# Kernel optimization log

Measured on AMD Instinct MI355X. Metric: run time of the kernel, lower is better.

The kernel has to match this reference:

```python
import jax, jax.numpy as jnp
import numpy as np

HID, FFN, NE, TOPK = 1024, 4096, 8, 2


def setup_inputs() -> dict:
    key = jax.random.key(0)
    ks = jax.random.split(key, 4)
    x = jax.random.normal(ks[0], (2, 2048, HID), dtype=jnp.float32)
    # router: nn.Linear(hidden, num_experts, bias=False), init std=0.02; stored as [H, E]
    Wr = jax.random.normal(ks[1], (HID, NE), dtype=jnp.float32) * 0.02
    # per-expert FFN weights stacked on leading expert axis
    W1 = jax.random.normal(ks[2], (NE, HID, FFN), dtype=jnp.float32) * (1.0 / np.sqrt(HID))
    b1 = jnp.zeros((NE, FFN), dtype=jnp.float32)
    W2 = jax.random.normal(ks[3], (NE, FFN, HID), dtype=jnp.float32) * (1.0 / np.sqrt(FFN))
    b2 = jnp.zeros((NE, HID), dtype=jnp.float32)
    return {"x": x, "Wr": Wr, "W1": W1, "b1": b1, "W2": W2, "b2": b2}


def reference(x, Wr, W1, b1, W2, b2):
    B, S, H = x.shape
    E = Wr.shape[1]
    T = B * S
    xf = x.reshape(T, H)                                  # [T, H]
    logits = xf @ Wr                                      # [T, E]
    probs = jax.nn.softmax(logits, axis=-1)
    topk_p, topk_i = jax.lax.top_k(probs, TOPK)           # [T, K]
    topk_p = topk_p / jnp.sum(topk_p, axis=-1, keepdims=True)
    # dense combine weights: c[t, e] = normalized prob if expert e selected for token t else 0
    c = jnp.zeros((T, E), dtype=xf.dtype).at[jnp.arange(T)[:, None], topk_i].add(topk_p)

    def expert_step(acc, ew):
        w1, bb1, w2, bb2, ce = ew                         # ce: [T]
        h = jax.nn.gelu(xf @ w1 + bb1, approximate=False)  # exact GELU like nn.GELU()
        y = h @ w2 + bb2                                  # [T, H]
        return acc + ce[:, None] * y, None

    out, _ = jax.lax.scan(expert_step, jnp.zeros_like(xf), (W1, b1, W2, b2, c.T))
    return out.reshape(B, S, H)
```

## Files before the change

### kernel.cpp

```cpp
#include <hip/hip_runtime.h>
#include <hip/hip_bf16.h>

#define H 1024
#define F 4096
#define NE 8
#define T 4096

typedef unsigned short u16;
typedef float floatx4 __attribute__((ext_vector_type(4)));
typedef short short8 __attribute__((ext_vector_type(8)));

__device__ __forceinline__ u16 f2bf(float f) {
  union { float f; unsigned int u; } c; c.f = f;
  unsigned int u = c.u;
  return (u16)((u + 0x7fffu + ((u >> 16) & 1u)) >> 16);
}

__device__ __forceinline__ void load16_lds(const u16* g, u16* l) {
  __builtin_amdgcn_global_load_lds(
      (const __attribute__((address_space(1))) unsigned int*)g,
      (__attribute__((address_space(3))) unsigned int*)l, 16, 0, 0);
}

__global__ __launch_bounds__(256) void router_kernel(
    const float* __restrict__ x, const float* __restrict__ Wr,
    int* __restrict__ cnt, int* __restrict__ tok, float* __restrict__ wgt) {
  int t = (blockIdx.x * 256 + threadIdx.x) >> 6;
  int lane = threadIdx.x & 63;
  const float* xr = x + (size_t)t * H;
  double p[NE];
#pragma unroll
  for (int e = 0; e < NE; ++e) p[e] = 0.0;
  for (int k = lane; k < H; k += 64) {
    float xv = xr[k];
    const float4* wr4 = reinterpret_cast<const float4*>(Wr + k * NE);
    float4 a = wr4[0], b = wr4[1];
    p[0] += (double)xv * a.x; p[1] += (double)xv * a.y;
    p[2] += (double)xv * a.z; p[3] += (double)xv * a.w;
    p[4] += (double)xv * b.x; p[5] += (double)xv * b.y;
    p[6] += (double)xv * b.z; p[7] += (double)xv * b.w;
  }
#pragma unroll
  for (int e = 0; e < NE; ++e) {
#pragma unroll
    for (int off = 32; off; off >>= 1) p[e] += __shfl_down(p[e], off, 64);
  }
  if (lane == 0) {
    int i0 = 0;
#pragma unroll
    for (int e = 1; e < NE; ++e) if (p[e] > p[i0]) i0 = e;
    int i1 = (i0 == 0) ? 1 : 0;
#pragma unroll
    for (int e = 0; e < NE; ++e) if (e != i0 && p[e] > p[i1]) i1 = e;
    double d = exp(p[i1] - p[i0]);
    float w0 = (float)(1.0 / (1.0 + d));
    float w1 = (float)(d / (1.0 + d));
    int pos0 = atomicAdd(&cnt[i0], 1);
    tok[i0 * T + pos0] = t; wgt[i0 * T + pos0] = w0;
    int pos1 = atomicAdd(&cnt[i1], 1);
    tok[i1 * T + pos1] = t; wgt[i1 * T + pos1] = w1;
  }
}

__global__ void offsets_kernel(const int* __restrict__ cnt, int* __restrict__ off) {
  if (threadIdx.x == 0) {
    int s = 0;
#pragma unroll
    for (int e = 0; e < NE; ++e) { off[e] = s; s += cnt[e]; }
    off[NE] = s;
  }
}

__global__ __launch_bounds__(256) void convert_x_kernel(
    const float* __restrict__ x, u16* __restrict__ xb) {
  int i = blockIdx.x * 256 + threadIdx.x;
  float4 v = reinterpret_cast<const float4*>(x)[i];
  ushort4 o;
  o.x = f2bf(v.x); o.y = f2bf(v.y); o.z = f2bf(v.z); o.w = f2bf(v.w);
  reinterpret_cast<ushort4*>(xb)[i] = o;
}

__global__ __launch_bounds__(256) void transpose_bf16_kernel(
    const float* __restrict__ src, u16* __restrict__ dst, int R, int C) {
  __shared__ u16 tile[64][72];
  int e = blockIdx.z;
  int c0 = blockIdx.x << 6, r0 = blockIdx.y << 6;
  const float* s = src + (size_t)e * R * C;
  u16* d = dst + (size_t)e * R * C;
  int t = threadIdx.x;
  int rl = t >> 4, cl = (t & 15) << 2;
#pragma unroll
  for (int i = 0; i < 4; ++i) {
    float4 v = *reinterpret_cast<const float4*>(&s[(size_t)(r0 + rl + i * 16) * C + c0 + cl]);
    ushort4 o; o.x = f2bf(v.x); o.y = f2bf(v.y); o.z = f2bf(v.z); o.w = f2bf(v.w);
    *reinterpret_cast<ushort4*>(&tile[rl + i * 16][cl]) = o;
  }
  __syncthreads();
  int cl2 = t >> 4, rl2 = (t & 15) << 2;
#pragma unroll
  for (int i = 0; i < 4; ++i) {
    ushort4 o;
    o.x = tile[rl2 + 0][cl2 + i * 16];
    o.y = tile[rl2 + 1][cl2 + i * 16];
    o.z = tile[rl2 + 2][cl2 + i * 16];
    o.w = tile[rl2 + 3][cl2 + i * 16];
    *reinterpret_cast<ushort4*>(&d[(size_t)(c0 + cl2 + i * 16) * R + r0 + rl2]) = o;
  }
}

__global__ __launch_bounds__(256) void gemm1_kernel(
    const u16* __restrict__ Xb, const u16* __restrict__ W1t,
    const float* __restrict__ b1, const int* __restrict__ cnt,
    const int* __restrict__ off, const int* __restrict__ tok,
    u16* __restrict__ Hc) {
  int e = blockIdx.z;
  int n = cnt[e];
  int m0 = blockIdx.y << 7;
  if (m0 >= n) return;
  int n0 = blockIdx.x << 7;
  int rb = off[e];

  __shared__ alignas(16) u16 As[128 * 32];
  __shared__ alignas(16) u16 Bs[128 * 32];
  __shared__ int tokS[128];

  int tid = threadIdx.x;
  if (tid < 128) {
    int s = m0 + tid;
    tokS[tid] = (s < n) ? tok[e * T + s] : 0;
  }
  __syncthreads();

  const u16* W1e = W1t + (size_t)e * F * H;
  const u16* aP0 = Xb + (size_t)tokS[tid >> 2] * H + (tid & 3) * 8;
  const u16* aP1 = Xb + (size_t)tokS[64 + (tid >> 2)] * H + (tid & 3) * 8;
  const u16* bP0 = W1e + (size_t)(n0 + (tid >> 2)) * H + (tid & 3) * 8;
  const u16* bP1 = W1e + (size_t)(n0 + 64 + (tid >> 2)) * H + (tid & 3) * 8;
  u16* aL0 = &As[tid * 8];        u16* aL1 = &As[(tid + 256) * 8];
  u16* bL0 = &Bs[tid * 8];        u16* bL1 = &Bs[(tid + 256) * 8];

  int wv = tid >> 6, lane = tid & 63;
  int wm = wv >> 1, wn = wv & 1;
  int quad = lane >> 4, l16 = lane & 15;

  floatx4 acc[4][4];
#pragma unroll
  for (int mt = 0; mt < 4; ++mt)
#pragma unroll
    for (int nt = 0; nt < 4; ++nt) acc[mt][nt] = floatx4{0.f, 0.f, 0.f, 0.f};

  const u16* aF[4]; const u16* bF[4];
#pragma unroll
  for (int i = 0; i < 4; ++i) {
    aF[i] = &As[(wm * 64 + i * 16 + l16) * 32 + quad * 8];
    bF[i] = &Bs[(wn * 64 + i * 16 + l16) * 32 + quad * 8];
  }

  for (int k0 = 0; k0 < H; k0 += 32) {
    load16_lds(aP0 + k0, aL0);
    load16_lds(aP1 + k0, aL1);
    load16_lds(bP0 + k0, bL0);
    load16_lds(bP1 + k0, bL1);
    __syncthreads();
    short8 av[4], bv[4];
#pragma unroll
    for (int i = 0; i < 4; ++i) {
      av[i] = *reinterpret_cast<const short8*>(aF[i]);
      bv[i] = *reinterpret_cast<const short8*>(bF[i]);
    }
#pragma unroll
    for (int mt = 0; mt < 4; ++mt)
#pragma unroll
      for (int nt = 0; nt < 4; ++nt)
        acc[mt][nt] = __builtin_amdgcn_mfma_f32_16x16x32_bf16(av[mt], bv[nt], acc[mt][nt], 0, 0, 0);
    __syncthreads();
  }

  float b1v[4];
#pragma unroll
  for (int nt = 0; nt < 4; ++nt)
    b1v[nt] = b1[e * F + n0 + wn * 64 + nt * 16 + l16];
#pragma unroll
  for (int mt = 0; mt < 4; ++mt) {
#pragma unroll
    for (int i = 0; i < 4; ++i) {
      int row = wm * 64 + mt * 16 + quad * 4 + i;
      int gr = m0 + row;
      if (gr < n) {
        u16* hrow = Hc + (size_t)(rb + gr) * F + n0 + wn * 64 + l16;
#pragma unroll
        for (int nt = 0; nt < 4; ++nt) {
          float v = acc[mt][nt][i] + b1v[nt];
          v = 0.5f * v * (1.0f + erff(v * 0.70710678118f));
          hrow[nt * 16] = f2bf(v);
        }
      }
    }
  }
}

__global__ __launch_bounds__(256) void gemm2_kernel(
    const u16* __restrict__ Hc, const u16* __restrict__ W2t,
    const float* __restrict__ b2, const int* __restrict__ cnt,
    const int* __restrict__ off, const int* __restrict__ tok,
    const float* __restrict__ wgt, float* __restrict__ out) {
  int e = blockIdx.z;
  int n = cnt[e];
  int m0 = blockIdx.y << 7;
  if (m0 >= n) return;
  int n0 = blockIdx.x << 7;
  int rb = off[e];

  __shared__ alignas(16) u16 As[128 * 32];
  __shared__ alignas(16) u16 Bs[128 * 32];

  int tid = threadIdx.x;
  const u16* W2e = W2t + (size_t)e * F * H;
  const u16* aP0 = Hc + (size_t)(rb + m0 + (tid >> 2)) * F + (tid & 3) * 8;
  const u16* aP1 = Hc + (size_t)(rb + m0 + 64 + (tid >> 2)) * F + (tid & 3) * 8;
  const u16* bP0 = W2e + (size_t)(n0 + (tid >> 2)) * F + (tid & 3) * 8;
  const u16* bP1 = W2e + (size_t)(n0 + 64 + (tid >> 2)) * F + (tid & 3) * 8;
  u16* aL0 = &As[tid * 8];        u16* aL1 = &As[(tid + 256) * 8];
  u16* bL0 = &Bs[tid * 8];        u16* bL1 = &Bs[(tid + 256) * 8];

  int wv = tid >> 6, lane = tid & 63;
  int wm = wv >> 1, wn = wv & 1;
  int quad = lane >> 4, l16 = lane & 15;

  floatx4 acc[4][4];
#pragma unroll
  for (int mt = 0; mt < 4; ++mt)
#pragma unroll
    for (int nt = 0; nt < 4; ++nt) acc[mt][nt] = floatx4{0.f, 0.f, 0.f, 0.f};

  const u16* aF[4]; const u16* bF[4];
#pragma unroll
  for (int i = 0; i < 4; ++i) {
    aF[i] = &As[(wm * 64 + i * 16 + l16) * 32 + quad * 8];
    bF[i] = &Bs[(wn * 64 + i * 16 + l16) * 32 + quad * 8];
  }

  for (int k0 = 0; k0 < F; k0 += 32) {
    load16_lds(aP0 + k0, aL0);
    load16_lds(aP1 + k0, aL1);
    load16_lds(bP0 + k0, bL0);
    load16_lds(bP1 + k0, bL1);
    __syncthreads();
    short8 av[4], bv[4];
#pragma unroll
    for (int i = 0; i < 4; ++i) {
      av[i] = *reinterpret_cast<const short8*>(aF[i]);
      bv[i] = *reinterpret_cast<const short8*>(bF[i]);
    }
#pragma unroll
    for (int mt = 0; mt < 4; ++mt)
#pragma unroll
      for (int nt = 0; nt < 4; ++nt)
        acc[mt][nt] = __builtin_amdgcn_mfma_f32_16x16x32_bf16(av[mt], bv[nt], acc[mt][nt], 0, 0, 0);
    __syncthreads();
  }

  float b2v[4];
#pragma unroll
  for (int nt = 0; nt < 4; ++nt)
    b2v[nt] = b2[e * H + n0 + wn * 64 + nt * 16 + l16];
#pragma unroll
  for (int mt = 0; mt < 4; ++mt) {
#pragma unroll
    for (int i = 0; i < 4; ++i) {
      int row = wm * 64 + mt * 16 + quad * 4 + i;
      int gr = m0 + row;
      if (gr < n) {
        float wv2 = wgt[e * T + gr];
        int tk = tok[e * T + gr];
        float* orow = out + (size_t)tk * H + n0 + wn * 64 + l16;
#pragma unroll
        for (int nt = 0; nt < 4; ++nt)
          atomicAdd(orow + nt * 16, (acc[mt][nt][i] + b2v[nt]) * wv2);
      }
    }
  }
}

extern "C" void kernel_launch(void* const* d_in, const int* in_sizes, int n_in,
                              void* d_out, int out_size, void* d_ws, size_t ws_size,
                              hipStream_t stream) {
  const float* x  = (const float*)d_in[0];
  const float* Wr = (const float*)d_in[1];
  const float* W1 = (const float*)d_in[2];
  const float* b1 = (const float*)d_in[3];
  const float* W2 = (const float*)d_in[4];
  const float* b2 = (const float*)d_in[5];
  float* out = (float*)d_out;

  char* ws = (char*)d_ws;
  int*   cnt = (int*)(ws + 0);
  int*   off = (int*)(ws + 256);
  int*   tok = (int*)(ws + 4096);
  float* wgt = (float*)(ws + 135168);
  u16*   Xb  = (u16*)(ws + 266240);
  u16*   W1t = (u16*)(ws + 8654848);
  u16*   W2t = (u16*)(ws + 75763712);
  u16*   Hc  = (u16*)(ws + 142872576);

  hipMemsetAsync(cnt, 0, 64, stream);
  hipMemsetAsync(out, 0, (size_t)out_size * sizeof(float), stream);

  router_kernel<<<dim3(T / 4), dim3(256), 0, stream>>>(x, Wr, cnt, tok, wgt);
  offsets_kernel<<<dim3(1), dim3(64), 0, stream>>>(cnt, off);
  convert_x_kernel<<<dim3((T * H / 4) / 256), dim3(256), 0, stream>>>(x, Xb);
  transpose_bf16_kernel<<<dim3(F / 64, H / 64, NE), dim3(256), 0, stream>>>(W1, W1t, H, F);
  transpose_bf16_kernel<<<dim3(H / 64, F / 64, NE), dim3(256), 0, stream>>>(W2, W2t, F, H);
  gemm1_kernel<<<dim3(F / 128, 32, NE), dim3(256), 0, stream>>>(Xb, W1t, b1, cnt, off, tok, Hc);
  gemm2_kernel<<<dim3(H / 128, 32, NE), dim3(256), 0, stream>>>(Hc, W2t, b2, cnt, off, tok, wgt, out);
}
```

Baseline: 699.5 us.

## Fuse x conversion into router, stage GEMM1 stores via LDS, split-K GEMM2

Converting x to bf16 now happens inside the router kernel, so the separate convert launch is gone. GEMM1's epilogue uses a tanh-style GELU approximation (sigmoid form with __expf and rcp) and writes its output through an LDS tile, which gives coalesced 16-byte stores instead of scattered 2-byte ones. GEMM2 splits K into two halves across grid z to double the block count, and both halves atomically add into the output. The GELU approximation departs from the exact erf form, and the split-K doubles the atomic traffic on the output.

```diff
diff --git a/kernel.cpp b/kernel.cpp
--- a/kernel.cpp
+++ b/kernel.cpp
@@ -16,6 +16,13 @@
   return (u16)((u + 0x7fffu + ((u >> 16) & 1u)) >> 16);
 }
 
+__device__ __forceinline__ float gelu_f(float x) {
+  float x3 = x * x * x;
+  float m2y = -1.5957691216f * x - 0.0713548162f * x3;
+  float u = __expf(m2y);
+  return x * __builtin_amdgcn_rcpf(1.0f + u);
+}
+
 __device__ __forceinline__ void load16_lds(const u16* g, u16* l) {
   __builtin_amdgcn_global_load_lds(
       (const __attribute__((address_space(1))) unsigned int*)g,
@@ -24,7 +31,8 @@
 
 __global__ __launch_bounds__(256) void router_kernel(
     const float* __restrict__ x, const float* __restrict__ Wr,
-    int* __restrict__ cnt, int* __restrict__ tok, float* __restrict__ wgt) {
+    int* __restrict__ cnt, int* __restrict__ tok, float* __restrict__ wgt,
+    u16* __restrict__ xb) {
   int t = (blockIdx.x * 256 + threadIdx.x) >> 6;
   int lane = threadIdx.x & 63;
   const float* xr = x + (size_t)t * H;
@@ -60,6 +68,15 @@
     int pos1 = atomicAdd(&cnt[i1], 1);
     tok[i1 * T + pos1] = t; wgt[i1 * T + pos1] = w1;
   }
+  const float4* xs4 = reinterpret_cast<const float4*>(x + (size_t)blockIdx.x * 4 * H);
+  ushort4* xd4 = reinterpret_cast<ushort4*>(xb + (size_t)blockIdx.x * 4 * H);
+#pragma unroll
+  for (int i = 0; i < 4; ++i) {
+    float4 v = xs4[threadIdx.x + i * 256];
+    ushort4 o;
+    o.x = f2bf(v.x); o.y = f2bf(v.y); o.z = f2bf(v.z); o.w = f2bf(v.w);
+    xd4[threadIdx.x + i * 256] = o;
+  }
 }
 
 __global__ void offsets_kernel(const int* __restrict__ cnt, int* __restrict__ off) {
@@ -69,15 +86,6 @@
     for (int e = 0; e < NE; ++e) { off[e] = s; s += cnt[e]; }
     off[NE] = s;
   }
-}
-
-__global__ __launch_bounds__(256) void convert_x_kernel(
-    const float* __restrict__ x, u16* __restrict__ xb) {
-  int i = blockIdx.x * 256 + threadIdx.x;
-  float4 v = reinterpret_cast<const float4*>(x)[i];
-  ushort4 o;
-  o.x = f2bf(v.x); o.y = f2bf(v.y); o.z = f2bf(v.z); o.w = f2bf(v.w);
-  reinterpret_cast<ushort4*>(xb)[i] = o;
 }
 
 __global__ __launch_bounds__(256) void transpose_bf16_kernel(
@@ -122,6 +130,7 @@
 
   __shared__ alignas(16) u16 As[128 * 32];
   __shared__ alignas(16) u16 Bs[128 * 32];
+  __shared__ alignas(16) u16 Cs[128][72];
   __shared__ int tokS[128];
 
   int tid = threadIdx.x;
@@ -180,21 +189,29 @@
 #pragma unroll
   for (int nt = 0; nt < 4; ++nt)
     b1v[nt] = b1[e * F + n0 + wn * 64 + nt * 16 + l16];
-#pragma unroll
-  for (int mt = 0; mt < 4; ++mt) {
-#pragma unroll
-    for (int i = 0; i < 4; ++i) {
-      int row = wm * 64 + mt * 16 + quad * 4 + i;
-      int gr = m0 + row;
-      if (gr < n) {
-        u16* hrow = Hc + (size_t)(rb + gr) * F + n0 + wn * 64 + l16;
-#pragma unroll
-        for (int nt = 0; nt < 4; ++nt) {
-          float v = acc[mt][nt][i] + b1v[nt];
-          v = 0.5f * v * (1.0f + erff(v * 0.70710678118f));
-          hrow[nt * 16] = f2bf(v);
+
+#pragma unroll
+  for (int p = 0; p < 2; ++p) {
+    __syncthreads();
+    if (wn == p) {
+#pragma unroll
+      for (int mt = 0; mt < 4; ++mt)
+#pragma unroll
+        for (int i = 0; i < 4; ++i) {
+          int row = wm * 64 + mt * 16 + quad * 4 + i;
+#pragma unroll
+          for (int nt = 0; nt < 4; ++nt)
+            Cs[row][nt * 16 + l16] = f2bf(gelu_f(acc[mt][nt][i] + b1v[nt]));
         }
-      }
+    }
+    __syncthreads();
+    int row = tid >> 1, c0 = (tid & 1) * 32;
+    if (m0 + row < n) {
+      u16* dst = Hc + (size_t)(rb + m0 + row) * F + n0 + p * 64 + c0;
+#pragma unroll
+      for (int j = 0; j < 4; ++j)
+        *reinterpret_cast<short8*>(dst + j * 8) =
+            *reinterpret_cast<const short8*>(&Cs[row][c0 + j * 8]);
     }
   }
 }
@@ -204,22 +221,24 @@
     const float* __restrict__ b2, const int* __restrict__ cnt,
     const int* __restrict__ off, const int* __restrict__ tok,
     const float* __restrict__ wgt, float* __restrict__ out) {
-  int e = blockIdx.z;
+  int e = blockIdx.z >> 1;
+  int kh = blockIdx.z & 1;
   int n = cnt[e];
   int m0 = blockIdx.y << 7;
   if (m0 >= n) return;
   int n0 = blockIdx.x << 7;
   int rb = off[e];
+  int kbase = kh * (F / 2);
 
   __shared__ alignas(16) u16 As[128 * 32];
   __shared__ alignas(16) u16 Bs[128 * 32];
 
   int tid = threadIdx.x;
   const u16* W2e = W2t + (size_t)e * F * H;
-  const u16* aP0 = Hc + (size_t)(rb + m0 + (tid >> 2)) * F + (tid & 3) * 8;
-  const u16* aP1 = Hc + (size_t)(rb + m0 + 64 + (tid >> 2)) * F + (tid & 3) * 8;
-  const u16* bP0 = W2e + (size_t)(n0 + (tid >> 2)) * F + (tid & 3) * 8;
-  const u16* bP1 = W2e + (size_t)(n0 + 64 + (tid >> 2)) * F + (tid & 3) * 8;
+  const u16* aP0 = Hc + (size_t)(rb + m0 + (tid >> 2)) * F + kbase + (tid & 3) * 8;
+  const u16* aP1 = Hc + (size_t)(rb + m0 + 64 + (tid >> 2)) * F + kbase + (tid & 3) * 8;
+  const u16* bP0 = W2e + (size_t)(n0 + (tid >> 2)) * F + kbase + (tid & 3) * 8;
+  const u16* bP1 = W2e + (size_t)(n0 + 64 + (tid >> 2)) * F + kbase + (tid & 3) * 8;
   u16* aL0 = &As[tid * 8];        u16* aL1 = &As[(tid + 256) * 8];
   u16* bL0 = &Bs[tid * 8];        u16* bL1 = &Bs[(tid + 256) * 8];
 
@@ -240,7 +259,7 @@
     bF[i] = &Bs[(wn * 64 + i * 16 + l16) * 32 + quad * 8];
   }
 
-  for (int k0 = 0; k0 < F; k0 += 32) {
+  for (int k0 = 0; k0 < F / 2; k0 += 32) {
     load16_lds(aP0 + k0, aL0);
     load16_lds(aP1 + k0, aL1);
     load16_lds(bP0 + k0, bL0);
@@ -263,7 +282,7 @@
   float b2v[4];
 #pragma unroll
   for (int nt = 0; nt < 4; ++nt)
-    b2v[nt] = b2[e * H + n0 + wn * 64 + nt * 16 + l16];
+    b2v[nt] = (kh == 0) ? b2[e * H + n0 + wn * 64 + nt * 16 + l16] : 0.0f;
 #pragma unroll
   for (int mt = 0; mt < 4; ++mt) {
 #pragma unroll
@@ -306,11 +325,10 @@
   hipMemsetAsync(cnt, 0, 64, stream);
   hipMemsetAsync(out, 0, (size_t)out_size * sizeof(float), stream);
 
-  router_kernel<<<dim3(T / 4), dim3(256), 0, stream>>>(x, Wr, cnt, tok, wgt);
+  router_kernel<<<dim3(T / 4), dim3(256), 0, stream>>>(x, Wr, cnt, tok, wgt, Xb);
   offsets_kernel<<<dim3(1), dim3(64), 0, stream>>>(cnt, off);
-  convert_x_kernel<<<dim3((T * H / 4) / 256), dim3(256), 0, stream>>>(x, Xb);
   transpose_bf16_kernel<<<dim3(F / 64, H / 64, NE), dim3(256), 0, stream>>>(W1, W1t, H, F);
   transpose_bf16_kernel<<<dim3(H / 64, F / 64, NE), dim3(256), 0, stream>>>(W2, W2t, F, H);
   gemm1_kernel<<<dim3(F / 128, 32, NE), dim3(256), 0, stream>>>(Xb, W1t, b1, cnt, off, tok, Hc);
-  gemm2_kernel<<<dim3(H / 128, 32, NE), dim3(256), 0, stream>>>(Hc, W2t, b2, cnt, off, tok, wgt, out);
-}
+  gemm2_kernel<<<dim3(H / 128, 32, NE * 2), dim3(256), 0, stream>>>(Hc, W2t, b2, cnt, off, tok, wgt, out);
+}
```

Result: slower. 724.1 us (+3.5%).
